# Performance work log

Measured on AMD Instinct MI355X. Metric: run time of the kernel, lower is better.

The kernel has to match this reference:

```python
import jax, jax.numpy as jnp
import numpy as np

# Dimensions: B batches, E links, T time steps, F flows, rank-r factors, K unrolled iters
B, E, T, F = 16, 256, 4096, 512
RANK = 10
NUM_ITER = 5


def setup_inputs() -> dict:
    key = jax.random.key(0)
    ks = jax.random.split(key, 9)
    Y = jax.random.normal(ks[0], (B, E, T), dtype=jnp.float32)
    R = (jax.random.uniform(ks[1], (B, E, F)) < 0.1).astype(jnp.float32)
    Omega = (jax.random.uniform(ks[2], (B, E, T)) < 0.9).astype(jnp.float32)
    P0 = jax.random.normal(ks[3], (B, E, RANK), dtype=jnp.float32) * 0.1
    Q0 = jax.random.normal(ks[4], (B, T, RANK), dtype=jnp.float32) * 0.1
    # per-iteration learned log-parameters of the unrolled network
    lam_log = jax.random.normal(ks[5], (NUM_ITER,), dtype=jnp.float32) * 0.1 - 1.0
    mu_log = jax.random.normal(ks[6], (NUM_ITER,), dtype=jnp.float32) * 0.1 - 1.0
    nu_log = jax.random.normal(ks[7], (NUM_ITER,), dtype=jnp.float32) * 0.1
    gamma_logit = jax.random.normal(ks[8], (NUM_ITER,), dtype=jnp.float32) * 0.1
    return {"Y": Y, "R": R, "Omega": Omega, "P0": P0, "Q0": Q0,
            "lam_log": lam_log, "mu_log": mu_log, "nu_log": nu_log,
            "gamma_logit": gamma_logit}


def reference(Y, R, Omega, P0, Q0, lam_log, mu_log, nu_log, gamma_logit):
    """Unrolled BSCA: Y ~ X + R @ A + noise on observed entries (Omega mask),
    X relaxed low-rank via factors P (B,E,r), Q (B,T,r); A sparse anomalies (B,F,T).
    Each iteration: rank-r ridge solves for P and Q (left=False -> rhs @ inv(lhs)),
    relaxed X update, soft-thresholded BSCA direction for A + convex-combination step."""
    rank = P0.shape[-1]
    eye = jnp.eye(rank, dtype=Y.dtype)
    X = Omega * Y                     # (B,E,T) init relaxed variable
    A = jnp.zeros((*Y.shape[:-2], R.shape[-1], Y.shape[-1]), dtype=Y.dtype)  # (B,F,T)
    P, Q = P0, Q0
    A_scale = (R * R).mT @ (Omega * Omega)          # (B,F,T)
    noobs = A_scale == 0
    A_scale_safe = A_scale + noobs.astype(Y.dtype)
    for k in range(NUM_ITER):
        lam = jnp.exp(lam_log[k])
        mu = jnp.exp(mu_log[k])
        nu = jnp.exp(nu_log[k])
        gamma = jax.nn.sigmoid(gamma_logit[k])
        regp = lam / nu
        # P update: P = (X @ Q) @ inv(Q^T Q + regp I)   (right solve; lhs symmetric)
        lhsQ = Q.mT @ Q + regp * eye                 # (B,r,r)
        P = jnp.linalg.solve(lhsQ, (X @ Q).mT).mT    # (B,E,r)
        # Q update: Q = (X^T @ P) @ inv(P^T P + regp I)
        lhsP = P.mT @ P + regp * eye
        Q = jnp.linalg.solve(lhsP, (X.mT @ P).mT).mT # (B,T,r)
        # X update (relaxed): X = (Omega*err + nu*P Q^T) / (Omega^2 + nu)
        RA = R @ A                                   # (B,E,T)
        err = Omega * (Y - RA)
        X = (Omega * err + nu * (P @ Q.mT)) / (Omega * Omega + nu)
        # A update: soft-thresholded best-response + convex combination step
        resid = Omega * (Y - X - RA)                 # (B,E,T)
        BA = A + (R.mT @ resid) / A_scale_safe       # (B,F,T)
        A_dir = jnp.sign(BA) * jnp.maximum(jnp.abs(BA) - mu / A_scale_safe, 0.0)
        A_dir = jnp.where(noobs, 0.0, A_dir)
        A = A + gamma * (A_dir - A)
    return A
```

## Files before the change

kernel.cpp:

```cpp
#include <hip/hip_runtime.h>
#include <stdint.h>

#define BB 16
#define EE 256
#define TT 4096
#define FF 512
#define RK 10
#define NIT 5

typedef short bf16x8 __attribute__((ext_vector_type(8)));
typedef float f32x4  __attribute__((ext_vector_type(4)));

__device__ __forceinline__ unsigned short f2bf(float x){
  unsigned int u = __float_as_uint(x);
  unsigned int r = (u + 0x7FFFu + ((u >> 16) & 1u)) >> 16;
  return (unsigned short)r;
}
__device__ __forceinline__ float bf2f(unsigned short s){
  return __uint_as_float(((unsigned int)s) << 16);
}

__device__ __forceinline__ void gld16(const void* g, void* l){
  __builtin_amdgcn_global_load_lds((const __attribute__((address_space(1))) unsigned int*)g,
                                   (__attribute__((address_space(3))) unsigned int*)l,
                                   16, 0, 0);
}


__global__ void k_params(const float* lam_log, const float* mu_log,
                         const float* nu_log, const float* gl, float* prm){
  int k = threadIdx.x;
  if (k < NIT){
    float lam = expf(lam_log[k]);
    float mu  = expf(mu_log[k]);
    float nu  = expf(nu_log[k]);
    float gam = 1.0f/(1.0f+expf(-gl[k]));
    prm[k*8+0]=lam; prm[k*8+1]=mu; prm[k*8+2]=nu; prm[k*8+3]=gam; prm[k*8+4]=lam/nu;
  }
}

__global__ void k_initX(const float4* __restrict__ Y, const float4* __restrict__ Om,
                        float4* __restrict__ X, ushort4* __restrict__ Omb){
  int i = blockIdx.x*256 + threadIdx.x;
  float4 y = Y[i], o = Om[i];
  X[i] = make_float4(y.x*o.x, y.y*o.y, y.z*o.z, y.w*o.w);
  ushort4 ob; ob.x=f2bf(o.x); ob.y=f2bf(o.y); ob.z=f2bf(o.z); ob.w=f2bf(o.w);
  Omb[i] = ob;
}

__global__ void k_qtrans(const float* __restrict__ Q0, float* __restrict__ Qt){
  int idx = blockIdx.x*256 + threadIdx.x;
  int b = idx >> 12, t = idx & (TT-1);
  #pragma unroll
  for (int j=0;j<RK;j++)
    Qt[((size_t)b*RK + j)*TT + t] = Q0[(size_t)idx*RK + j];
}

__global__ void k_rtrans(const float* __restrict__ Rm, float* __restrict__ Rt){
  int f = blockIdx.x, b = blockIdx.y, e = threadIdx.x;
  Rt[((size_t)b*FF + f)*EE + e] = Rm[((size_t)b*EE + e)*FF + f];
}

__global__ void k_rbf(const float4* __restrict__ R, ushort4* __restrict__ Rb){
  int i = blockIdx.x*256 + threadIdx.x;
  float4 v = R[i];
  ushort4 o; o.x=f2bf(v.x); o.y=f2bf(v.y); o.z=f2bf(v.z); o.w=f2bf(v.w);
  Rb[i] = o;
}

__global__ void k_ascale(const float* __restrict__ Rt, const unsigned short* __restrict__ Omb,
                         unsigned short* __restrict__ As){
  int id = blockIdx.x;
  int xcd = id & 7;
  int within = id >> 3;
  int f = within & (FF-1);
  int g = ((within >> 9) << 3) + xcd;
  int b = g >> 2;
  int t = (g & 3)*1024 + threadIdx.x*4;
  __shared__ int s_cnt;
  __shared__ short s_idx[EE];
  __shared__ float s_w[EE];
  if (threadIdx.x==0) s_cnt = 0;
  __syncthreads();
  {
    int e = threadIdx.x;
    float w = Rt[((size_t)b*FF + f)*EE + e];
    if (w != 0.0f){ int p = atomicAdd(&s_cnt,1); s_idx[p]=(short)e; s_w[p]=w*w; }
  }
  __syncthreads();
  int cnt = s_cnt;
  float4 acc = {0,0,0,0};
  const unsigned short* Ob = Omb + (size_t)b*EE*TT + t;
  for (int it=0; it<cnt; ++it){
    int e = s_idx[it]; float w2 = s_w[it];
    ushort4 ou = *(const ushort4*)(Ob + (size_t)e*TT);
    float ox=bf2f(ou.x), oy=bf2f(ou.y), oz=bf2f(ou.z), ow=bf2f(ou.w);
    acc.x += w2*ox*ox; acc.y += w2*oy*oy; acc.z += w2*oz*oz; acc.w += w2*ow*ow;
  }
  ushort4 r; r.x=f2bf(acc.x); r.y=f2bf(acc.y); r.z=f2bf(acc.z); r.w=f2bf(acc.w);
  *(ushort4*)(As + ((size_t)b*FF + f)*TT + t) = r;
}


__global__ void k_lhsQ(const float* __restrict__ Qt, const float* __restrict__ prm,
                       float* __restrict__ lhs, int k){
  int p = blockIdx.x, b = blockIdx.y;
  int i = 0, rem = p;
  while (rem >= i+1){ rem -= (i+1); ++i; }
  int j = rem;
  const float* qi = Qt + ((size_t)b*RK + i)*TT;
  const float* qj = Qt + ((size_t)b*RK + j)*TT;
  float a = 0.0f;
  for (int t = threadIdx.x*4; t < TT; t += 1024){
    float4 x = *(const float4*)(qi+t);
    float4 y = *(const float4*)(qj+t);
    a += x.x*y.x + x.y*y.y + x.z*y.z + x.w*y.w;
  }
  __shared__ float red[256];
  red[threadIdx.x] = a; __syncthreads();
  for (int s=128; s>0; s>>=1){
    if (threadIdx.x < s) red[threadIdx.x] += red[threadIdx.x+s];
    __syncthreads();
  }
  if (threadIdx.x==0){
    float v = red[0];
    if (i==j) v += prm[k*8+4];
    lhs[(b*RK+i)*RK + j] = v;
    lhs[(b*RK+j)*RK + i] = v;
  }
}

__global__ void k_lhsP(const float* __restrict__ P, const float* __restrict__ prm,
                       float* __restrict__ lhs, int k){
  int p = blockIdx.x, b = blockIdx.y;
  int i = 0, rem = p;
  while (rem >= i+1){ rem -= (i+1); ++i; }
  int j = rem;
  int e = threadIdx.x;
  const float* pr = P + ((size_t)b*EE + e)*RK;
  float a = pr[i]*pr[j];
  __shared__ float red[256];
  red[threadIdx.x] = a; __syncthreads();
  for (int s=128; s>0; s>>=1){
    if (threadIdx.x < s) red[threadIdx.x] += red[threadIdx.x+s];
    __syncthreads();
  }
  if (threadIdx.x==0){
    float v = red[0];
    if (i==j) v += prm[k*8+4];
    lhs[(b*RK+i)*RK + j] = v;
    lhs[(b*RK+j)*RK + i] = v;
  }
}

__global__ void k_invert(const float* __restrict__ lhs, float* __restrict__ inv){
  int b = blockIdx.x;
  __shared__ float aug[RK][2*RK];
  int tid = threadIdx.x;
  int i = tid / (2*RK), j = tid % (2*RK);
  bool act = tid < RK*2*RK;
  if (act) aug[i][j] = (j < RK) ? lhs[(b*RK+i)*RK + j] : ((j-RK)==i ? 1.0f : 0.0f);
  __syncthreads();
  for (int kk=0; kk<RK; ++kk){
    float pinv = 1.0f / aug[kk][kk];
    __syncthreads();
    if (act && i==kk) aug[i][j] *= pinv;
    __syncthreads();
    float factor = (act && i!=kk) ? aug[i][kk] : 0.0f;
    float pivrow = act ? aug[kk][j] : 0.0f;
    __syncthreads();
    if (act && i!=kk) aug[i][j] -= factor * pivrow;
    __syncthreads();
  }
  if (act && j >= RK) inv[(b*RK+i)*RK + (j-RK)] = aug[i][j];
}

__global__ void k_Pupd(const float* __restrict__ X, const float* __restrict__ Qt,
                       const float* __restrict__ inv, float* __restrict__ P){
  int e = blockIdx.x, b = blockIdx.y;
  const float* xr = X + ((size_t)b*EE + e)*TT;
  const float* qb = Qt + (size_t)b*RK*TT;
  float acc[RK];
  #pragma unroll
  for (int j=0;j<RK;j++) acc[j]=0.0f;
  for (int t = threadIdx.x*4; t < TT; t += 1024){
    float4 x = *(const float4*)(xr+t);
    #pragma unroll
    for (int j=0;j<RK;j++){
      float4 q = *(const float4*)(qb + (size_t)j*TT + t);
      acc[j] += x.x*q.x + x.y*q.y + x.z*q.z + x.w*q.w;
    }
  }
  __shared__ float partial[4][RK];
  int lane = threadIdx.x & 63, wv = threadIdx.x >> 6;
  #pragma unroll
  for (int j=0;j<RK;j++){
    float v = acc[j];
    for (int s=32;s>0;s>>=1) v += __shfl_down(v, s, 64);
    if (lane==0) partial[wv][j] = v;
  }
  __syncthreads();
  if (threadIdx.x < RK){
    int i = threadIdx.x;
    float out = 0.0f;
    #pragma unroll
    for (int j=0;j<RK;j++){
      float xq = partial[0][j]+partial[1][j]+partial[2][j]+partial[3][j];
      out += xq * inv[(b*RK+j)*RK + i];
    }
    P[((size_t)b*EE + e)*RK + i] = out;
  }
}

__global__ void k_Qupd(const float* __restrict__ X, const float* __restrict__ P,
                       const float* __restrict__ inv, float* __restrict__ Qt){
  int b = blockIdx.y;
  int t = blockIdx.x*256 + threadIdx.x;
  __shared__ float sP[EE*RK];
  __shared__ float sInv[RK*RK];
  for (int i=threadIdx.x; i<EE*RK; i+=256) sP[i] = P[(size_t)b*EE*RK + i];
  if (threadIdx.x < RK*RK) sInv[threadIdx.x] = inv[b*RK*RK + threadIdx.x];
  __syncthreads();
  float acc[RK];
  #pragma unroll
  for (int j=0;j<RK;j++) acc[j]=0.0f;
  const float* xb = X + (size_t)b*EE*TT + t;
  for (int e=0;e<EE;e++){
    float x = xb[(size_t)e*TT];
    #pragma unroll
    for (int j=0;j<RK;j++) acc[j] += x * sP[e*RK+j];
  }
  #pragma unroll
  for (int i=0;i<RK;i++){
    float q = 0.0f;
    #pragma unroll
    for (int j=0;j<RK;j++) q += acc[j]*sInv[j*RK+i];
    Qt[((size_t)b*RK + i)*TT + t] = q;
  }
}

__global__ void k_atrans(const float* __restrict__ A, unsigned short* __restrict__ Abt){
  __shared__ float sT[64][65];
  int b  = blockIdx.z;
  int F0 = blockIdx.y*64, T0 = blockIdx.x*64;
  int tid = threadIdx.x;
  int fi = tid >> 4;
  int m  = tid & 15;
  #pragma unroll
  for (int pass=0; pass<4; ++pass){
    int f = pass*16 + fi;
    float4 v = *(const float4*)(A + ((size_t)(b*FF + F0 + f))*TT + T0 + m*4);
    sT[f][m*4+0]=v.x; sT[f][m*4+1]=v.y; sT[f][m*4+2]=v.z; sT[f][m*4+3]=v.w;
  }
  __syncthreads();
  #pragma unroll
  for (int pass=0; pass<4; ++pass){
    int t  = pass*16 + fi;
    int f4 = m*4;
    ushort4 o;
    o.x = f2bf(sT[f4+0][t]); o.y = f2bf(sT[f4+1][t]);
    o.z = f2bf(sT[f4+2][t]); o.w = f2bf(sT[f4+3][t]);
    *(ushort4*)(Abt + ((size_t)b*TT + T0 + t)*FF + F0 + f4) = o;
  }
}

__global__ __launch_bounds__(256) void k_gemm1m(
    const unsigned short* __restrict__ Rb, const unsigned short* __restrict__ Abt,
    const float* __restrict__ Y, const unsigned short* __restrict__ Omb,
    const float* __restrict__ Qt, const float* __restrict__ P,
    const float* __restrict__ prm, float* __restrict__ X,
    unsigned short* __restrict__ resid, int k)
{
  __shared__ __align__(16) unsigned char lds[16384];
  int id = blockIdx.x;
  int b  = id >> 6;
  int e0 = ((id >> 5) & 1) * 128;
  int t0 = (id & 31) * 128;
  int tid  = threadIdx.x;
  int lane = tid & 63, wid = tid >> 6;
  int lr = lane & 15, lg = lane >> 4;
  int wm = wid >> 1, wn = wid & 1;

  f32x4 acc[4][4];
  #pragma unroll
  for (int m=0;m<4;++m)
    #pragma unroll
    for (int n=0;n<4;++n)
      #pragma unroll
      for (int i=0;i<4;++i) acc[m][n][i]=0.0f;

  if (k > 0){
    int swz  = ((lg ^ (lr & 3)) << 4);
    int aoff = (wm*64 + lr)*64 + swz;
    int boff = 8192 + (wn*64 + lr)*64 + swz;
    int c0 = tid, c1 = tid + 256;
    int r0 = c0 >> 2, s0 = c0 & 3;
    int r1 = c1 >> 2, s1 = c1 & 3;
    const unsigned short* gA0 = Rb  + ((size_t)(b*EE + e0 + r0))*FF + ((s0 ^ (r0&3))<<3);
    const unsigned short* gA1 = Rb  + ((size_t)(b*EE + e0 + r1))*FF + ((s1 ^ (r1&3))<<3);
    const unsigned short* gB0 = Abt + ((size_t)b*TT + t0 + r0)*FF   + ((s0 ^ (r0&3))<<3);
    const unsigned short* gB1 = Abt + ((size_t)b*TT + t0 + r1)*FF   + ((s1 ^ (r1&3))<<3);
    unsigned char* lA0 = lds + c0*16;
    unsigned char* lA1 = lds + c1*16;
    unsigned char* lB0 = lds + 8192 + c0*16;
    unsigned char* lB1 = lds + 8192 + c1*16;

    for (int kk=0; kk<16; ++kk){
      __syncthreads();
      int f0 = kk*32;
      gld16(gA0 + f0, lA0);
      gld16(gA1 + f0, lA1);
      gld16(gB0 + f0, lB0);
      gld16(gB1 + f0, lB1);
      asm volatile("s_waitcnt vmcnt(0)" ::: "memory");
      __syncthreads();
      bf16x8 af[4], bb[4];
      #pragma unroll
      for (int m=0;m<4;++m) af[m] = *(const bf16x8*)(lds + aoff + m*1024);
      #pragma unroll
      for (int n=0;n<4;++n) bb[n] = *(const bf16x8*)(lds + boff + n*1024);
      #pragma unroll
      for (int m=0;m<4;++m)
        #pragma unroll
        for (int n=0;n<4;++n)
          acc[m][n] = __builtin_amdgcn_mfma_f32_16x16x32_bf16(af[m], bb[n], acc[m][n], 0, 0, 0);
    }
  }

  __syncthreads();
  float* Pl = (float*)lds;
  float* Ql = (float*)(lds + 8192);
  for (int idx = tid; idx < 128*RK; idx += 256)
    Pl[idx] = P[((size_t)(b*EE + e0))*RK + idx];
  for (int idx = tid; idx < RK*128; idx += 256){
    int j = idx >> 7, t = idx & 127;
    Ql[idx] = Qt[((size_t)(b*RK + j))*TT + t0 + t];
  }
  __syncthreads();

  float nu = prm[k*8+2];
  #pragma unroll
  for (int m=0;m<4;++m){
    #pragma unroll
    for (int r=0;r<4;++r){
      int eloc = wm*64 + m*16 + lg*4 + r;
      float pv[RK];
      #pragma unroll
      for (int j=0;j<RK;++j) pv[j] = Pl[eloc*RK + j];
      size_t rowoff = ((size_t)(b*EE + e0 + eloc))*TT + t0;
      #pragma unroll
      for (int n=0;n<4;++n){
        int tloc = wn*64 + n*16 + lr;
        float ra = acc[m][n][r];
        float pq = 0.0f;
        #pragma unroll
        for (int j=0;j<RK;++j) pq += pv[j]*Ql[j*128 + tloc];
        size_t off = rowoff + tloc;
        float y = Y[off];
        float o = bf2f(Omb[off]);
        float d = y - ra, om2 = o*o;
        float x = (om2*d + nu*pq)/(om2 + nu);
        float rs = o*(y - x - ra);
        X[off] = x;
        resid[off] = f2bf(rs);
      }
    }
  }
}

__device__ __forceinline__ float aupd(float a, float g, unsigned short asu,
                                      float mu, float gamma){
  float as = bf2f(asu);
  bool no = (as == 0.0f);
  float rs = 1.0f / (no ? 1.0f : as);
  float ba = a + g*rs;
  float ad = copysignf(fmaxf(fabsf(ba) - mu*rs, 0.0f), ba);
  if (no) ad = 0.0f;
  return a + gamma*(ad - a);
}

__global__ void k_gemm2(const float* __restrict__ Rt, const unsigned short* __restrict__ resid,
                        const unsigned short* __restrict__ As,
                        const float* __restrict__ prm, float* __restrict__ A, int k){
  int id = blockIdx.x;
  int xcd = id & 7;
  int within = id >> 3;
  int f = within & (FF-1);
  int g = ((within >> 9) << 3) + xcd;
  int b = g >> 2;
  int t = (g & 3)*1024 + threadIdx.x*4;
  __shared__ int s_cnt;
  __shared__ short s_idx[EE];
  __shared__ float s_w[EE];
  if (threadIdx.x==0) s_cnt = 0;
  __syncthreads();
  {
    int e = threadIdx.x;
    float w = Rt[((size_t)b*FF + f)*EE + e];
    if (w != 0.0f){ int p = atomicAdd(&s_cnt,1); s_idx[p]=(short)e; s_w[p]=w; }
  }
  __syncthreads();
  int cnt = s_cnt;
  float4 gacc = {0,0,0,0};
  const unsigned short* rb = resid + (size_t)b*EE*TT + t;
  for (int it=0; it<cnt; ++it){
    int e = s_idx[it]; float w = s_w[it];
    ushort4 r4 = *(const ushort4*)(rb + (size_t)e*TT);
    gacc.x += w*bf2f(r4.x); gacc.y += w*bf2f(r4.y);
    gacc.z += w*bf2f(r4.z); gacc.w += w*bf2f(r4.w);
  }
  float mu = prm[k*8+1], gamma = prm[k*8+3];
  size_t off = ((size_t)b*FF + f)*TT + t;
  ushort4 asv = *(const ushort4*)(As + off);
  float4 a = *(float4*)(A + off);
  float4 an;
  an.x = aupd(a.x, gacc.x, asv.x, mu, gamma);
  an.y = aupd(a.y, gacc.y, asv.y, mu, gamma);
  an.z = aupd(a.z, gacc.z, asv.z, mu, gamma);
  an.w = aupd(a.w, gacc.w, asv.w, mu, gamma);
  *(float4*)(A + off) = an;
}


extern "C" void kernel_launch(void* const* d_in, const int* in_sizes, int n_in,
                              void* d_out, int out_size, void* d_ws, size_t ws_size,
                              hipStream_t stream){
  const float* Y   = (const float*)d_in[0];
  const float* Rm  = (const float*)d_in[1];
  const float* Om  = (const float*)d_in[2];
  const float* P0  = (const float*)d_in[3];
  const float* Q0  = (const float*)d_in[4];
  const float* lam = (const float*)d_in[5];
  const float* mu  = (const float*)d_in[6];
  const float* nu  = (const float*)d_in[7];
  const float* gl  = (const float*)d_in[8];
  float* A = (float*)d_out;

  char* ws = (char*)d_ws;
  const size_t X_OFF   = 0;
  const size_t RES_OFF = X_OFF   + (size_t)BB*EE*TT*4;
  const size_t OMB_OFF = RES_OFF + (size_t)BB*EE*TT*2;
  const size_t AS_OFF  = OMB_OFF + (size_t)BB*EE*TT*2;
  const size_t RT_OFF  = AS_OFF  + (size_t)BB*FF*TT*2;
  const size_t QT_OFF  = RT_OFF  + (size_t)BB*FF*EE*4;
  const size_t P_OFF   = QT_OFF  + (size_t)BB*RK*TT*4;
  const size_t LHS_OFF = P_OFF   + (size_t)BB*EE*RK*4;
  const size_t INV_OFF = LHS_OFF + (size_t)BB*RK*RK*4;
  const size_t PRM_OFF = INV_OFF + (size_t)BB*RK*RK*4;
  const size_t RB_OFF  = PRM_OFF + 4096;
  const size_t ABT_OFF = RB_OFF  + (size_t)BB*EE*FF*2;

  float* X    = (float*)(ws + X_OFF);
  unsigned short* resid = (unsigned short*)(ws + RES_OFF);
  unsigned short* Omb   = (unsigned short*)(ws + OMB_OFF);
  unsigned short* As    = (unsigned short*)(ws + AS_OFF);
  float* Rt   = (float*)(ws + RT_OFF);
  float* Qt   = (float*)(ws + QT_OFF);
  float* P    = (float*)(ws + P_OFF);
  float* lhs  = (float*)(ws + LHS_OFF);
  float* inv  = (float*)(ws + INV_OFF);
  float* prm  = (float*)(ws + PRM_OFF);
  unsigned short* Rb  = (unsigned short*)(ws + RB_OFF);
  unsigned short* Abt = (unsigned short*)(ws + ABT_OFF);

  (void)P0; (void)Om; (void)in_sizes; (void)n_in; (void)ws_size;

  hipMemsetAsync(d_out, 0, (size_t)out_size*sizeof(float), stream);
  k_params<<<1, 64, 0, stream>>>(lam, mu, nu, gl, prm);
  k_initX<<<BB*EE*TT/4/256, 256, 0, stream>>>((const float4*)Y, (const float4*)Om,
                                              (float4*)X, (ushort4*)Omb);
  k_qtrans<<<BB*TT/256, 256, 0, stream>>>(Q0, Qt);
  k_rtrans<<<dim3(FF, BB), 256, 0, stream>>>(Rm, Rt);
  k_rbf<<<BB*EE*FF/4/256, 256, 0, stream>>>((const float4*)Rm, (ushort4*)Rb);
  k_ascale<<<FF*4*BB, 256, 0, stream>>>(Rt, Omb, As);

  for (int k=0; k<NIT; ++k){
    k_lhsQ  <<<dim3(55, BB), 256, 0, stream>>>(Qt, prm, lhs, k);
    k_invert<<<BB, 256, 0, stream>>>(lhs, inv);
    k_Pupd  <<<dim3(EE, BB), 256, 0, stream>>>(X, Qt, inv, P);
    k_lhsP  <<<dim3(55, BB), 256, 0, stream>>>(P, prm, lhs, k);
    k_invert<<<BB, 256, 0, stream>>>(lhs, inv);
    k_Qupd  <<<dim3(TT/256, BB), 256, 0, stream>>>(X, P, inv, Qt);
    if (k > 0)
      k_atrans<<<dim3(TT/64, FF/64, BB), 256, 0, stream>>>(A, Abt);
    k_gemm1m<<<BB*2*32, 256, 0, stream>>>(Rb, Abt, Y, Omb, Qt, P, prm, X, resid, k);
    k_gemm2 <<<FF*4*BB, 256, 0, stream>>>(Rt, resid, As, prm, A, k);
  }
}
```

Before: 2.106 ms.

## Replace sparse gather R^T@resid and A_scale with bf16 MFMA GEMMs

The sparse-gather kernels for R^T @ resid and for A_scale are replaced with dense bf16 MFMA GEMM kernels. These use LDS tiling and read transposed bf16 copies of R, Omega and the residual. gemm1m now writes the residual transposed through a per-wave LDS staging buffer so the second GEMM can load it with contiguous K. This trades the sparse skip of zero links (about 10% density) for dense matrix-core throughput, and adds transpose kernels and extra workspace.

```diff
diff --git a/kernel.cpp b/kernel.cpp
--- a/kernel.cpp
+++ b/kernel.cpp
@@ -56,11 +56,6 @@
     Qt[((size_t)b*RK + j)*TT + t] = Q0[(size_t)idx*RK + j];
 }
 
-__global__ void k_rtrans(const float* __restrict__ Rm, float* __restrict__ Rt){
-  int f = blockIdx.x, b = blockIdx.y, e = threadIdx.x;
-  Rt[((size_t)b*FF + f)*EE + e] = Rm[((size_t)b*EE + e)*FF + f];
-}
-
 __global__ void k_rbf(const float4* __restrict__ R, ushort4* __restrict__ Rb){
   int i = blockIdx.x*256 + threadIdx.x;
   float4 v = R[i];
@@ -68,37 +63,35 @@
   Rb[i] = o;
 }
 
-__global__ void k_ascale(const float* __restrict__ Rt, const unsigned short* __restrict__ Omb,
-                         unsigned short* __restrict__ As){
-  int id = blockIdx.x;
-  int xcd = id & 7;
-  int within = id >> 3;
-  int f = within & (FF-1);
-  int g = ((within >> 9) << 3) + xcd;
-  int b = g >> 2;
-  int t = (g & 3)*1024 + threadIdx.x*4;
-  __shared__ int s_cnt;
-  __shared__ short s_idx[EE];
-  __shared__ float s_w[EE];
-  if (threadIdx.x==0) s_cnt = 0;
+__global__ void k_rtransb(const float* __restrict__ Rm, unsigned short* __restrict__ Rbt){
+  int f = blockIdx.x, b = blockIdx.y, e = threadIdx.x;
+  Rbt[((size_t)b*FF + f)*EE + e] = f2bf(Rm[((size_t)b*EE + e)*FF + f]);
+}
+
+__global__ void k_omtrans(const unsigned short* __restrict__ Omb,
+                          unsigned short* __restrict__ OmbT){
+  __shared__ unsigned short sT[64][66];
+  int b  = blockIdx.z;
+  int E0 = blockIdx.y*64, T0 = blockIdx.x*64;
+  int tid = threadIdx.x;
+  int fi = tid >> 4;
+  int m  = tid & 15;
+  #pragma unroll
+  for (int pass=0; pass<4; ++pass){
+    int e = pass*16 + fi;
+    ushort4 v = *(const ushort4*)(Omb + ((size_t)(b*EE + E0 + e))*TT + T0 + m*4);
+    sT[e][m*4+0]=v.x; sT[e][m*4+1]=v.y; sT[e][m*4+2]=v.z; sT[e][m*4+3]=v.w;
+  }
   __syncthreads();
-  {
-    int e = threadIdx.x;
-    float w = Rt[((size_t)b*FF + f)*EE + e];
-    if (w != 0.0f){ int p = atomicAdd(&s_cnt,1); s_idx[p]=(short)e; s_w[p]=w*w; }
-  }
-  __syncthreads();
-  int cnt = s_cnt;
-  float4 acc = {0,0,0,0};
-  const unsigned short* Ob = Omb + (size_t)b*EE*TT + t;
-  for (int it=0; it<cnt; ++it){
-    int e = s_idx[it]; float w2 = s_w[it];
-    ushort4 ou = *(const ushort4*)(Ob + (size_t)e*TT);
-    float ox=bf2f(ou.x), oy=bf2f(ou.y), oz=bf2f(ou.z), ow=bf2f(ou.w);
-    acc.x += w2*ox*ox; acc.y += w2*oy*oy; acc.z += w2*oz*oz; acc.w += w2*ow*ow;
-  }
-  ushort4 r; r.x=f2bf(acc.x); r.y=f2bf(acc.y); r.z=f2bf(acc.z); r.w=f2bf(acc.w);
-  *(ushort4*)(As + ((size_t)b*FF + f)*TT + t) = r;
+  #pragma unroll
+  for (int pass=0; pass<4; ++pass){
+    int t  = pass*16 + fi;
+    int e4 = m*4;
+    ushort4 o;
+    o.x = sT[e4+0][t]; o.y = sT[e4+1][t];
+    o.z = sT[e4+2][t]; o.w = sT[e4+3][t];
+    *(ushort4*)(OmbT + ((size_t)b*TT + T0 + t)*EE + E0 + e4) = o;
+  }
 }
 
 
@@ -269,9 +262,9 @@
     const float* __restrict__ Y, const unsigned short* __restrict__ Omb,
     const float* __restrict__ Qt, const float* __restrict__ P,
     const float* __restrict__ prm, float* __restrict__ X,
-    unsigned short* __restrict__ resid, int k)
+    unsigned short* __restrict__ residT, int k)
 {
-  __shared__ __align__(16) unsigned char lds[16384];
+  __shared__ __align__(16) unsigned char lds[20480];
   int id = blockIdx.x;
   int b  = id >> 6;
   int e0 = ((id >> 5) & 1) * 128;
@@ -328,8 +321,9 @@
   }
 
   __syncthreads();
-  float* Pl = (float*)lds;
-  float* Ql = (float*)(lds + 8192);
+  unsigned short* wbuf = (unsigned short*)(lds + wid*2176);
+  float* Pl = (float*)(lds + 8704);
+  float* Ql = (float*)(lds + 8704 + 5120);
   for (int idx = tid; idx < 128*RK; idx += 256)
     Pl[idx] = P[((size_t)(b*EE + e0))*RK + idx];
   for (int idx = tid; idx < RK*128; idx += 256){
@@ -340,31 +334,40 @@
 
   float nu = prm[k*8+2];
   #pragma unroll
-  for (int m=0;m<4;++m){
-    #pragma unroll
-    for (int r=0;r<4;++r){
-      int eloc = wm*64 + m*16 + lg*4 + r;
-      float pv[RK];
-      #pragma unroll
-      for (int j=0;j<RK;++j) pv[j] = Pl[eloc*RK + j];
-      size_t rowoff = ((size_t)(b*EE + e0 + eloc))*TT + t0;
-      #pragma unroll
-      for (int n=0;n<4;++n){
-        int tloc = wn*64 + n*16 + lr;
-        float ra = acc[m][n][r];
+  for (int n=0;n<4;++n){
+    int tloc = wn*64 + n*16 + lr;
+    float ql[RK];
+    #pragma unroll
+    for (int j=0;j<RK;++j) ql[j] = Ql[j*128 + tloc];
+    asm volatile("" ::: "memory");
+    #pragma unroll
+    for (int m=0;m<4;++m){
+      #pragma unroll
+      for (int r=0;r<4;++r){
+        int eloc = wm*64 + m*16 + lg*4 + r;
         float pq = 0.0f;
         #pragma unroll
-        for (int j=0;j<RK;++j) pq += pv[j]*Ql[j*128 + tloc];
-        size_t off = rowoff + tloc;
+        for (int j=0;j<RK;++j) pq += Pl[eloc*RK + j]*ql[j];
+        float ra = acc[m][n][r];
+        size_t off = ((size_t)(b*EE + e0 + eloc))*TT + t0 + tloc;
         float y = Y[off];
         float o = bf2f(Omb[off]);
         float d = y - ra, om2 = o*o;
         float x = (om2*d + nu*pq)/(om2 + nu);
         float rs = o*(y - x - ra);
         X[off] = x;
-        resid[off] = f2bf(rs);
+        wbuf[lr*68 + m*16 + lg*4 + r] = f2bf(rs);
       }
     }
+    asm volatile("" ::: "memory");
+    #pragma unroll
+    for (int j2=0;j2<4;++j2){
+      int row = j2*4 + lg;
+      int c4  = lr*4;
+      ushort4 vv = *(const ushort4*)(wbuf + row*68 + c4);
+      *(ushort4*)(residT + ((size_t)b*TT + t0 + wn*64 + n*16 + row)*EE + e0 + wm*64 + c4) = vv;
+    }
+    asm volatile("" ::: "memory");
   }
 }
 
@@ -379,46 +382,154 @@
   return a + gamma*(ad - a);
 }
 
-__global__ void k_gemm2(const float* __restrict__ Rt, const unsigned short* __restrict__ resid,
-                        const unsigned short* __restrict__ As,
-                        const float* __restrict__ prm, float* __restrict__ A, int k){
+__global__ __launch_bounds__(256) void k_gemm2m(
+    const unsigned short* __restrict__ Rbt, const unsigned short* __restrict__ residT,
+    const unsigned short* __restrict__ As, const float* __restrict__ prm,
+    float* __restrict__ A, int k)
+{
+  __shared__ __align__(16) unsigned char lds[16384];
   int id = blockIdx.x;
-  int xcd = id & 7;
-  int within = id >> 3;
-  int f = within & (FF-1);
-  int g = ((within >> 9) << 3) + xcd;
-  int b = g >> 2;
-  int t = (g & 3)*1024 + threadIdx.x*4;
-  __shared__ int s_cnt;
-  __shared__ short s_idx[EE];
-  __shared__ float s_w[EE];
-  if (threadIdx.x==0) s_cnt = 0;
-  __syncthreads();
-  {
-    int e = threadIdx.x;
-    float w = Rt[((size_t)b*FF + f)*EE + e];
-    if (w != 0.0f){ int p = atomicAdd(&s_cnt,1); s_idx[p]=(short)e; s_w[p]=w; }
-  }
-  __syncthreads();
-  int cnt = s_cnt;
-  float4 gacc = {0,0,0,0};
-  const unsigned short* rb = resid + (size_t)b*EE*TT + t;
-  for (int it=0; it<cnt; ++it){
-    int e = s_idx[it]; float w = s_w[it];
-    ushort4 r4 = *(const ushort4*)(rb + (size_t)e*TT);
-    gacc.x += w*bf2f(r4.x); gacc.y += w*bf2f(r4.y);
-    gacc.z += w*bf2f(r4.z); gacc.w += w*bf2f(r4.w);
-  }
+  int b  = id >> 7;
+  int f0 = ((id >> 5) & 3) * 128;
+  int t0 = (id & 31) * 128;
+  int tid  = threadIdx.x;
+  int lane = tid & 63, wid = tid >> 6;
+  int lr = lane & 15, lg = lane >> 4;
+  int wm = wid >> 1, wn = wid & 1;
+
+  f32x4 acc[4][4];
+  #pragma unroll
+  for (int m=0;m<4;++m)
+    #pragma unroll
+    for (int n=0;n<4;++n)
+      #pragma unroll
+      for (int i=0;i<4;++i) acc[m][n][i]=0.0f;
+
+  int swz  = ((lg ^ (lr & 3)) << 4);
+  int aoff = (wm*64 + lr)*64 + swz;
+  int boff = 8192 + (wn*64 + lr)*64 + swz;
+  int c0 = tid, c1 = tid + 256;
+  int r0 = c0 >> 2, s0 = c0 & 3;
+  int r1 = c1 >> 2, s1 = c1 & 3;
+  const unsigned short* gA0 = Rbt    + ((size_t)(b*FF + f0 + r0))*EE + ((s0 ^ (r0&3))<<3);
+  const unsigned short* gA1 = Rbt    + ((size_t)(b*FF + f0 + r1))*EE + ((s1 ^ (r1&3))<<3);
+  const unsigned short* gB0 = residT + ((size_t)b*TT + t0 + r0)*EE   + ((s0 ^ (r0&3))<<3);
+  const unsigned short* gB1 = residT + ((size_t)b*TT + t0 + r1)*EE   + ((s1 ^ (r1&3))<<3);
+  unsigned char* lA0 = lds + c0*16;
+  unsigned char* lA1 = lds + c1*16;
+  unsigned char* lB0 = lds + 8192 + c0*16;
+  unsigned char* lB1 = lds + 8192 + c1*16;
+
+  for (int kk=0; kk<8; ++kk){
+    __syncthreads();
+    int eoff = kk*32;
+    gld16(gA0 + eoff, lA0);
+    gld16(gA1 + eoff, lA1);
+    gld16(gB0 + eoff, lB0);
+    gld16(gB1 + eoff, lB1);
+    asm volatile("s_waitcnt vmcnt(0)" ::: "memory");
+    __syncthreads();
+    bf16x8 af[4], bb[4];
+    #pragma unroll
+    for (int m=0;m<4;++m) af[m] = *(const bf16x8*)(lds + aoff + m*1024);
+    #pragma unroll
+    for (int n=0;n<4;++n) bb[n] = *(const bf16x8*)(lds + boff + n*1024);
+    #pragma unroll
+    for (int m=0;m<4;++m)
+      #pragma unroll
+      for (int n=0;n<4;++n)
+        acc[m][n] = __builtin_amdgcn_mfma_f32_16x16x32_bf16(af[m], bb[n], acc[m][n], 0, 0, 0);
+  }
+
   float mu = prm[k*8+1], gamma = prm[k*8+3];
-  size_t off = ((size_t)b*FF + f)*TT + t;
-  ushort4 asv = *(const ushort4*)(As + off);
-  float4 a = *(float4*)(A + off);
-  float4 an;
-  an.x = aupd(a.x, gacc.x, asv.x, mu, gamma);
-  an.y = aupd(a.y, gacc.y, asv.y, mu, gamma);
-  an.z = aupd(a.z, gacc.z, asv.z, mu, gamma);
-  an.w = aupd(a.w, gacc.w, asv.w, mu, gamma);
-  *(float4*)(A + off) = an;
+  #pragma unroll
+  for (int m=0;m<4;++m){
+    #pragma unroll
+    for (int r=0;r<4;++r){
+      int floc = wm*64 + m*16 + lg*4 + r;
+      size_t rowoff = ((size_t)(b*FF + f0 + floc))*TT + t0;
+      #pragma unroll
+      for (int n=0;n<4;++n){
+        int tloc = wn*64 + n*16 + lr;
+        size_t off = rowoff + tloc;
+        float a = A[off];
+        A[off] = aupd(a, acc[m][n][r], As[off], mu, gamma);
+      }
+    }
+  }
+}
+
+__global__ __launch_bounds__(256) void k_ascalem(
+    const unsigned short* __restrict__ Rbt, const unsigned short* __restrict__ OmbT,
+    unsigned short* __restrict__ As)
+{
+  __shared__ __align__(16) unsigned char lds[16384];
+  int id = blockIdx.x;
+  int b  = id >> 7;
+  int f0 = ((id >> 5) & 3) * 128;
+  int t0 = (id & 31) * 128;
+  int tid  = threadIdx.x;
+  int lane = tid & 63, wid = tid >> 6;
+  int lr = lane & 15, lg = lane >> 4;
+  int wm = wid >> 1, wn = wid & 1;
+
+  f32x4 acc[4][4];
+  #pragma unroll
+  for (int m=0;m<4;++m)
+    #pragma unroll
+    for (int n=0;n<4;++n)
+      #pragma unroll
+      for (int i=0;i<4;++i) acc[m][n][i]=0.0f;
+
+  int swz  = ((lg ^ (lr & 3)) << 4);
+  int aoff = (wm*64 + lr)*64 + swz;
+  int boff = 8192 + (wn*64 + lr)*64 + swz;
+  int c0 = tid, c1 = tid + 256;
+  int r0 = c0 >> 2, s0 = c0 & 3;
+  int r1 = c1 >> 2, s1 = c1 & 3;
+  const unsigned short* gA0 = Rbt  + ((size_t)(b*FF + f0 + r0))*EE + ((s0 ^ (r0&3))<<3);
+  const unsigned short* gA1 = Rbt  + ((size_t)(b*FF + f0 + r1))*EE + ((s1 ^ (r1&3))<<3);
+  const unsigned short* gB0 = OmbT + ((size_t)b*TT + t0 + r0)*EE   + ((s0 ^ (r0&3))<<3);
+  const unsigned short* gB1 = OmbT + ((size_t)b*TT + t0 + r1)*EE   + ((s1 ^ (r1&3))<<3);
+  unsigned char* lA0 = lds + c0*16;
+  unsigned char* lA1 = lds + c1*16;
+  unsigned char* lB0 = lds + 8192 + c0*16;
+  unsigned char* lB1 = lds + 8192 + c1*16;
+
+  for (int kk=0; kk<8; ++kk){
+    __syncthreads();
+    int eoff = kk*32;
+    gld16(gA0 + eoff, lA0);
+    gld16(gA1 + eoff, lA1);
+    gld16(gB0 + eoff, lB0);
+    gld16(gB1 + eoff, lB1);
+    asm volatile("s_waitcnt vmcnt(0)" ::: "memory");
+    __syncthreads();
+    bf16x8 af[4], bb[4];
+    #pragma unroll
+    for (int m=0;m<4;++m) af[m] = *(const bf16x8*)(lds + aoff + m*1024);
+    #pragma unroll
+    for (int n=0;n<4;++n) bb[n] = *(const bf16x8*)(lds + boff + n*1024);
+    #pragma unroll
+    for (int m=0;m<4;++m)
+      #pragma unroll
+      for (int n=0;n<4;++n)
+        acc[m][n] = __builtin_amdgcn_mfma_f32_16x16x32_bf16(af[m], bb[n], acc[m][n], 0, 0, 0);
+  }
+
+  #pragma unroll
+  for (int m=0;m<4;++m){
+    #pragma unroll
+    for (int r=0;r<4;++r){
+      int floc = wm*64 + m*16 + lg*4 + r;
+      size_t rowoff = ((size_t)(b*FF + f0 + floc))*TT + t0;
+      #pragma unroll
+      for (int n=0;n<4;++n){
+        int tloc = wn*64 + n*16 + lr;
+        As[rowoff + tloc] = f2bf(acc[m][n][r]);
+      }
+    }
+  }
 }
 
 
@@ -437,31 +548,33 @@
   float* A = (float*)d_out;
 
   char* ws = (char*)d_ws;
-  const size_t X_OFF   = 0;
-  const size_t RES_OFF = X_OFF   + (size_t)BB*EE*TT*4;
-  const size_t OMB_OFF = RES_OFF + (size_t)BB*EE*TT*2;
-  const size_t AS_OFF  = OMB_OFF + (size_t)BB*EE*TT*2;
-  const size_t RT_OFF  = AS_OFF  + (size_t)BB*FF*TT*2;
-  const size_t QT_OFF  = RT_OFF  + (size_t)BB*FF*EE*4;
-  const size_t P_OFF   = QT_OFF  + (size_t)BB*RK*TT*4;
-  const size_t LHS_OFF = P_OFF   + (size_t)BB*EE*RK*4;
-  const size_t INV_OFF = LHS_OFF + (size_t)BB*RK*RK*4;
-  const size_t PRM_OFF = INV_OFF + (size_t)BB*RK*RK*4;
-  const size_t RB_OFF  = PRM_OFF + 4096;
-  const size_t ABT_OFF = RB_OFF  + (size_t)BB*EE*FF*2;
+  const size_t X_OFF    = 0;
+  const size_t REST_OFF = X_OFF    + (size_t)BB*EE*TT*4;
+  const size_t OMB_OFF  = REST_OFF + (size_t)BB*TT*EE*2;
+  const size_t AS_OFF   = OMB_OFF  + (size_t)BB*EE*TT*2;
+  const size_t QT_OFF   = AS_OFF   + (size_t)BB*FF*TT*2;
+  const size_t P_OFF    = QT_OFF   + (size_t)BB*RK*TT*4;
+  const size_t LHS_OFF  = P_OFF    + (size_t)BB*EE*RK*4;
+  const size_t INV_OFF  = LHS_OFF  + (size_t)BB*RK*RK*4;
+  const size_t PRM_OFF  = INV_OFF  + (size_t)BB*RK*RK*4;
+  const size_t RB_OFF   = PRM_OFF  + 4096;
+  const size_t RBT_OFF  = RB_OFF   + (size_t)BB*EE*FF*2;
+  const size_t OMBT_OFF = RBT_OFF  + (size_t)BB*FF*EE*2;
+  const size_t ABT_OFF  = OMBT_OFF + (size_t)BB*TT*EE*2;
 
   float* X    = (float*)(ws + X_OFF);
-  unsigned short* resid = (unsigned short*)(ws + RES_OFF);
-  unsigned short* Omb   = (unsigned short*)(ws + OMB_OFF);
-  unsigned short* As    = (unsigned short*)(ws + AS_OFF);
-  float* Rt   = (float*)(ws + RT_OFF);
+  unsigned short* residT = (unsigned short*)(ws + REST_OFF);
+  unsigned short* Omb    = (unsigned short*)(ws + OMB_OFF);
+  unsigned short* As     = (unsigned short*)(ws + AS_OFF);
   float* Qt   = (float*)(ws + QT_OFF);
   float* P    = (float*)(ws + P_OFF);
   float* lhs  = (float*)(ws + LHS_OFF);
   float* inv  = (float*)(ws + INV_OFF);
   float* prm  = (float*)(ws + PRM_OFF);
-  unsigned short* Rb  = (unsigned short*)(ws + RB_OFF);
-  unsigned short* Abt = (unsigned short*)(ws + ABT_OFF);
+  unsigned short* Rb   = (unsigned short*)(ws + RB_OFF);
+  unsigned short* Rbt  = (unsigned short*)(ws + RBT_OFF);
+  unsigned short* OmbT = (unsigned short*)(ws + OMBT_OFF);
+  unsigned short* Abt  = (unsigned short*)(ws + ABT_OFF);
 
   (void)P0; (void)Om; (void)in_sizes; (void)n_in; (void)ws_size;
 
@@ -470,9 +583,10 @@
   k_initX<<<BB*EE*TT/4/256, 256, 0, stream>>>((const float4*)Y, (const float4*)Om,
                                               (float4*)X, (ushort4*)Omb);
   k_qtrans<<<BB*TT/256, 256, 0, stream>>>(Q0, Qt);
-  k_rtrans<<<dim3(FF, BB), 256, 0, stream>>>(Rm, Rt);
   k_rbf<<<BB*EE*FF/4/256, 256, 0, stream>>>((const float4*)Rm, (ushort4*)Rb);
-  k_ascale<<<FF*4*BB, 256, 0, stream>>>(Rt, Omb, As);
+  k_rtransb<<<dim3(FF, BB), 256, 0, stream>>>(Rm, Rbt);
+  k_omtrans<<<dim3(TT/64, EE/64, BB), 256, 0, stream>>>(Omb, OmbT);
+  k_ascalem<<<2048, 256, 0, stream>>>(Rbt, OmbT, As);
 
   for (int k=0; k<NIT; ++k){
     k_lhsQ  <<<dim3(55, BB), 256, 0, stream>>>(Qt, prm, lhs, k);
@@ -483,7 +597,7 @@
     k_Qupd  <<<dim3(TT/256, BB), 256, 0, stream>>>(X, P, inv, Qt);
     if (k > 0)
       k_atrans<<<dim3(TT/64, FF/64, BB), 256, 0, stream>>>(A, Abt);
-    k_gemm1m<<<BB*2*32, 256, 0, stream>>>(Rb, Abt, Y, Omb, Qt, P, prm, X, resid, k);
-    k_gemm2 <<<FF*4*BB, 256, 0, stream>>>(Rt, resid, As, prm, A, k);
-  }
-}
+    k_gemm1m<<<BB*2*32, 256, 0, stream>>>(Rb, Abt, Y, Omb, Qt, P, prm, X, residT, k);
+    k_gemm2m<<<2048, 256, 0, stream>>>(Rbt, residT, As, prm, A, k);
+  }
+}
```

Measured after the change: 1.993 ms. -5.3%, faster.
